# Performance work log

Hardware: AMD Instinct MI355X
Metric: run time of the kernel (lower is better)

Reference implementation:

```python
import jax, jax.numpy as jnp
import numpy as np
import math

B, SQ, SK, D = 16, 2048, 2048, 64


def setup_inputs() -> dict:
    key = jax.random.key(0)
    kq, kk, kv, kl = jax.random.split(key, 4)
    queries = jax.random.normal(kq, (B, SQ, D), dtype=jnp.float32)
    keys = jax.random.normal(kk, (B, SK, D), dtype=jnp.float32)
    values = jax.random.normal(kv, (B, SK, D), dtype=jnp.float32)
    # valid key lengths in [1, SK]
    valid_lens = jax.random.randint(kl, (B,), 1, SK + 1, dtype=jnp.int32)
    return {"queries": queries, "keys": keys, "values": values, "valid_lens": valid_lens}


def reference(queries, keys, values, valid_lens):
    d = queries.shape[-1]
    # [B, SQ, SK] raw scores
    scores = jnp.einsum("bqd,bkd->bqk", queries, keys) / math.sqrt(d)
    # masked_softmax: key positions >= valid_len are set to -1e6 (d2l semantics)
    kpos = jnp.arange(scores.shape[-1], dtype=jnp.int32)  # [SK]
    mask = kpos[None, None, :] < valid_lens[:, None, None]  # [B,1,SK] -> broadcast
    scores = jnp.where(mask, scores, jnp.float32(-1e6))
    attn = jax.nn.softmax(scores, axis=-1)
    # dropout rate is 0.0 -> identity
    return jnp.einsum("bqk,bkd->bqd", attn, values)
```

## Files before the change

kernel.cpp:

```cpp
#include <hip/hip_runtime.h>

#define NB 16
#define SQL 2048
#define SKL 2048
#define DH 64

typedef __attribute__((ext_vector_type(8))) short bf16x8;
typedef __attribute__((ext_vector_type(4))) unsigned short u16x4;
typedef __attribute__((ext_vector_type(8))) unsigned short u16x8;
typedef __attribute__((ext_vector_type(4))) float f32x4;

#define LOG2E 1.4426950408889634f
#define K1 (0.125f * LOG2E)

__device__ __forceinline__ unsigned short f2bf(float f) {
    unsigned int u = __builtin_bit_cast(unsigned int, f);
    u += 0x7fffu + ((u >> 16) & 1u);
    return (unsigned short)(u >> 16);
}

__global__ __launch_bounds__(256) void prep_kernel(
    const float* __restrict__ Q, const float* __restrict__ K,
    const float* __restrict__ V,
    unsigned short* __restrict__ Qb, unsigned short* __restrict__ Kb,
    unsigned short* __restrict__ Vt) {
    const int blk = blockIdx.x;
    if (blk < 2048) {
        const float* src = (blk < 1024) ? Q : K;
        unsigned short* dst = (blk < 1024) ? Qb : Kb;
        const size_t base = ((size_t)(blk & 1023) * 256 + threadIdx.x) * 8;
        float4 a = *(const float4*)(src + base);
        float4 b = *(const float4*)(src + base + 4);
        u16x8 o;
        o[0] = f2bf(a.x); o[1] = f2bf(a.y); o[2] = f2bf(a.z); o[3] = f2bf(a.w);
        o[4] = f2bf(b.x); o[5] = f2bf(b.y); o[6] = f2bf(b.z); o[7] = f2bf(b.w);
        *(u16x8*)(dst + base) = o;
    } else {
        const int t  = blk - 2048;
        const int b  = t >> 5;
        const int kb = (t & 31) << 6;
        __shared__ float tile[64][65];
        const int tid = threadIdx.x;
        {
            const int r  = tid >> 2;
            const int cg = (tid & 3) << 4;
            const float* vsrc = V + ((size_t)b * SKL + (kb + r)) * DH;
            #pragma unroll
            for (int i = 0; i < 4; ++i) {
                float4 x = *(const float4*)(vsrc + cg + i * 4);
                tile[r][cg + i*4 + 0] = x.x;
                tile[r][cg + i*4 + 1] = x.y;
                tile[r][cg + i*4 + 2] = x.z;
                tile[r][cg + i*4 + 3] = x.w;
            }
        }
        __syncthreads();
        {
            const int d  = tid >> 2;
            const int kg = (tid & 3) << 4;
            unsigned short* dst = Vt + ((size_t)b * DH + d) * SKL + kb + kg;
            u16x8 o0, o1;
            #pragma unroll
            for (int j = 0; j < 8; ++j) o0[j] = f2bf(tile[kg + j][d]);
            #pragma unroll
            for (int j = 0; j < 8; ++j) o1[j] = f2bf(tile[kg + 8 + j][d]);
            *(u16x8*)(dst)     = o0;
            *(u16x8*)(dst + 8) = o1;
        }
    }
}

__global__ __launch_bounds__(256, 2) void attn_kernel(
    const unsigned short* __restrict__ Qb,
    const unsigned short* __restrict__ Kb,
    const unsigned short* __restrict__ Vt,
    const int* __restrict__ valid_lens,
    float* __restrict__ out) {
    const int b    = blockIdx.y;
    const int qblk = blockIdx.x;
    const int tid  = threadIdx.x;
    const int wave = tid >> 6;
    const int lane = tid & 63;
    const int c16  = lane & 15;
    const int quad = lane >> 4;

    const int valid  = valid_lens[b];
    const int ntiles = (valid + 63) >> 6;

    __shared__ unsigned short Klds[64][72];
    __shared__ unsigned short Vlds[64][72];
    __shared__ unsigned short Plds[4][16][72];

    const int q0 = qblk * 64 + wave * 16;
    const unsigned short* qptr = Qb + ((size_t)b * SQL + q0 + c16) * DH;
    const bf16x8 qf0 = *(const bf16x8*)(qptr + quad * 8);
    const bf16x8 qf1 = *(const bf16x8*)(qptr + 32 + quad * 8);

    const unsigned short* kbase = Kb + (size_t)b * SKL * DH;
    const unsigned short* vbase = Vt + (size_t)b * DH * SKL;

    const f32x4 zero = {0.f, 0.f, 0.f, 0.f};
    f32x4 o[4];
    #pragma unroll
    for (int i = 0; i < 4; ++i) o[i] = zero;
    float mrow = -1e30f, lrow = 0.f;

    for (int kt = 0; kt < ntiles; ++kt) {
        const int kb = kt << 6;
        #pragma unroll
        for (int i = 0; i < 2; ++i) {
            const int c   = i * 256 + tid;
            const int r   = c >> 3;
            const int col = (c & 7) << 3;
            *(u16x8*)&Klds[r][col] = *(const u16x8*)(kbase + (size_t)(kb + r) * DH + col);
            *(u16x8*)&Vlds[r][col] = *(const u16x8*)(vbase + (size_t)r * SKL + kb + col);
        }
        __syncthreads();

        f32x4 s[4];
        #pragma unroll
        for (int t = 0; t < 4; ++t) {
            s[t] = zero;
            const bf16x8 kf0 = *(const bf16x8*)&Klds[t * 16 + c16][quad * 8];
            const bf16x8 kf1 = *(const bf16x8*)&Klds[t * 16 + c16][32 + quad * 8];
            s[t] = __builtin_amdgcn_mfma_f32_16x16x32_bf16(kf0, qf0, s[t], 0, 0, 0);
            s[t] = __builtin_amdgcn_mfma_f32_16x16x32_bf16(kf1, qf1, s[t], 0, 0, 0);
        }

        if (kb + 64 > valid) {
            #pragma unroll
            for (int t = 0; t < 4; ++t)
                #pragma unroll
                for (int r = 0; r < 4; ++r)
                    if (kb + t * 16 + quad * 4 + r >= valid) s[t][r] = -1e30f;
        }

        float tmax = -1e30f;
        #pragma unroll
        for (int t = 0; t < 4; ++t)
            #pragma unroll
            for (int r = 0; r < 4; ++r) tmax = fmaxf(tmax, s[t][r]);
        tmax = fmaxf(tmax, __shfl_xor(tmax, 16));
        tmax = fmaxf(tmax, __shfl_xor(tmax, 32));

        const float mnew  = fmaxf(mrow, 0.125f * tmax);
        const float alpha = exp2f((mrow - mnew) * LOG2E);
        const float mk    = mnew * LOG2E;
        float rs = 0.f;
        #pragma unroll
        for (int t = 0; t < 4; ++t)
            #pragma unroll
            for (int r = 0; r < 4; ++r) {
                const float p = exp2f(fmaf(s[t][r], K1, -mk));
                s[t][r] = p;
                rs += p;
            }
        rs += __shfl_xor(rs, 16);
        rs += __shfl_xor(rs, 32);
        lrow = lrow * alpha + rs;
        mrow = mnew;
        #pragma unroll
        for (int i = 0; i < 4; ++i) o[i] *= alpha;

        #pragma unroll
        for (int t = 0; t < 4; ++t) {
            u16x4 pw;
            pw[0] = f2bf(s[t][0]); pw[1] = f2bf(s[t][1]);
            pw[2] = f2bf(s[t][2]); pw[3] = f2bf(s[t][3]);
            *(u16x4*)&Plds[wave][c16][t * 16 + quad * 4] = pw;
        }
        const bf16x8 pf0 = *(const bf16x8*)&Plds[wave][c16][quad * 8];
        const bf16x8 pf1 = *(const bf16x8*)&Plds[wave][c16][32 + quad * 8];

        #pragma unroll
        for (int dt = 0; dt < 4; ++dt) {
            const bf16x8 vf0 = *(const bf16x8*)&Vlds[dt * 16 + c16][quad * 8];
            const bf16x8 vf1 = *(const bf16x8*)&Vlds[dt * 16 + c16][32 + quad * 8];
            o[dt] = __builtin_amdgcn_mfma_f32_16x16x32_bf16(vf0, pf0, o[dt], 0, 0, 0);
            o[dt] = __builtin_amdgcn_mfma_f32_16x16x32_bf16(vf1, pf1, o[dt], 0, 0, 0);
        }
        __syncthreads();
    }

    const float inv = 1.0f / lrow;
    float* op = out + ((size_t)b * SQL + q0 + c16) * DH + quad * 4;
    #pragma unroll
    for (int dt = 0; dt < 4; ++dt) {
        f32x4 ov = o[dt] * inv;
        *(f32x4*)(op + dt * 16) = ov;
    }
}

extern "C" void kernel_launch(void* const* d_in, const int* in_sizes, int n_in,
                              void* d_out, int out_size, void* d_ws, size_t ws_size,
                              hipStream_t stream) {
    const float* Q  = (const float*)d_in[0];
    const float* K  = (const float*)d_in[1];
    const float* V  = (const float*)d_in[2];
    const int*   vl = (const int*)d_in[3];
    float* out = (float*)d_out;

    unsigned short* Qb = (unsigned short*)d_ws;
    unsigned short* Kb = Qb + (size_t)NB * SQL * DH;
    unsigned short* Vt = Kb + (size_t)NB * SKL * DH;

    prep_kernel<<<dim3(2560), dim3(256), 0, stream>>>(Q, K, V, Qb, Kb, Vt);
    attn_kernel<<<dim3(SQL / 64, NB), dim3(256), 0, stream>>>(Qb, Kb, Vt, vl, out);
}
```

Baseline: 119.3 us.

## Split attention over key chunks with a separate reduce kernel, add prefetch and LDS swizzle

```diff
diff --git a/kernel.cpp b/kernel.cpp
--- a/kernel.cpp
+++ b/kernel.cpp
@@ -4,6 +4,8 @@
 #define SQL 2048
 #define SKL 2048
 #define DH 64
+#define NSPLIT 4
+#define CHUNK 512
 
 typedef __attribute__((ext_vector_type(8))) short bf16x8;
 typedef __attribute__((ext_vector_type(4))) unsigned short u16x4;
@@ -70,26 +72,33 @@
     }
 }
 
-__global__ __launch_bounds__(256, 2) void attn_kernel(
+__global__ __launch_bounds__(256, 4) void attn_kernel(
     const unsigned short* __restrict__ Qb,
     const unsigned short* __restrict__ Kb,
     const unsigned short* __restrict__ Vt,
     const int* __restrict__ valid_lens,
-    float* __restrict__ out) {
-    const int b    = blockIdx.y;
-    const int qblk = blockIdx.x;
+    float* __restrict__ Opart,
+    float2* __restrict__ MLpart) {
+    const int qblk  = blockIdx.x;
+    const int split = blockIdx.y;
+    const int b     = blockIdx.z;
+
+    const int valid  = valid_lens[b];
+    const int kstart = split * CHUNK;
+    if (kstart >= valid) return;
+    const int kend   = (valid < kstart + CHUNK) ? valid : (kstart + CHUNK);
+    const int ntiles = (kend - kstart + 63) >> 6;
+
     const int tid  = threadIdx.x;
     const int wave = tid >> 6;
     const int lane = tid & 63;
     const int c16  = lane & 15;
     const int quad = lane >> 4;
-
-    const int valid  = valid_lens[b];
-    const int ntiles = (valid + 63) >> 6;
-
-    __shared__ unsigned short Klds[64][72];
-    __shared__ unsigned short Vlds[64][72];
-    __shared__ unsigned short Plds[4][16][72];
+    const int h    = c16 & 7;
+
+    __shared__ unsigned short Klds[64][64];
+    __shared__ unsigned short Vlds[64][64];
+    __shared__ unsigned short Plds[4][16][64];
 
     const int q0 = qblk * 64 + wave * 16;
     const unsigned short* qptr = Qb + ((size_t)b * SQL + q0 + c16) * DH;
@@ -105,34 +114,53 @@
     for (int i = 0; i < 4; ++i) o[i] = zero;
     float mrow = -1e30f, lrow = 0.f;
 
+    u16x8 kreg[2], vreg[2];
+    {
+        #pragma unroll
+        for (int i = 0; i < 2; ++i) {
+            const int c = i * 256 + tid, r = c >> 3, col = (c & 7) << 3;
+            kreg[i] = *(const u16x8*)(kbase + (size_t)(kstart + r) * DH + col);
+            vreg[i] = *(const u16x8*)(vbase + (size_t)r * SKL + kstart + col);
+        }
+    }
+
     for (int kt = 0; kt < ntiles; ++kt) {
-        const int kb = kt << 6;
+        const int kb = kstart + (kt << 6);
+        __syncthreads();
         #pragma unroll
         for (int i = 0; i < 2; ++i) {
-            const int c   = i * 256 + tid;
-            const int r   = c >> 3;
-            const int col = (c & 7) << 3;
-            *(u16x8*)&Klds[r][col] = *(const u16x8*)(kbase + (size_t)(kb + r) * DH + col);
-            *(u16x8*)&Vlds[r][col] = *(const u16x8*)(vbase + (size_t)r * SKL + kb + col);
+            const int c = i * 256 + tid, r = c >> 3;
+            const int pc = ((c & 7) ^ (r & 7)) << 3;
+            *(u16x8*)&Klds[r][pc] = kreg[i];
+            *(u16x8*)&Vlds[r][pc] = vreg[i];
         }
         __syncthreads();
+        if (kt + 1 < ntiles) {
+            const int kn = kb + 64;
+            #pragma unroll
+            for (int i = 0; i < 2; ++i) {
+                const int c = i * 256 + tid, r = c >> 3, col = (c & 7) << 3;
+                kreg[i] = *(const u16x8*)(kbase + (size_t)(kn + r) * DH + col);
+                vreg[i] = *(const u16x8*)(vbase + (size_t)r * SKL + kn + col);
+            }
+        }
 
         f32x4 s[4];
         #pragma unroll
         for (int t = 0; t < 4; ++t) {
             s[t] = zero;
-            const bf16x8 kf0 = *(const bf16x8*)&Klds[t * 16 + c16][quad * 8];
-            const bf16x8 kf1 = *(const bf16x8*)&Klds[t * 16 + c16][32 + quad * 8];
+            const bf16x8 kf0 = *(const bf16x8*)&Klds[t*16 + c16][(quad       ^ h) << 3];
+            const bf16x8 kf1 = *(const bf16x8*)&Klds[t*16 + c16][((quad + 4) ^ h) << 3];
             s[t] = __builtin_amdgcn_mfma_f32_16x16x32_bf16(kf0, qf0, s[t], 0, 0, 0);
             s[t] = __builtin_amdgcn_mfma_f32_16x16x32_bf16(kf1, qf1, s[t], 0, 0, 0);
         }
 
-        if (kb + 64 > valid) {
+        if (kb + 64 > kend) {
             #pragma unroll
             for (int t = 0; t < 4; ++t)
                 #pragma unroll
                 for (int r = 0; r < 4; ++r)
-                    if (kb + t * 16 + quad * 4 + r >= valid) s[t][r] = -1e30f;
+                    if (kb + t * 16 + quad * 4 + r >= kend) s[t][r] = -1e30f;
         }
 
         float tmax = -1e30f;
@@ -167,28 +195,59 @@
             u16x4 pw;
             pw[0] = f2bf(s[t][0]); pw[1] = f2bf(s[t][1]);
             pw[2] = f2bf(s[t][2]); pw[3] = f2bf(s[t][3]);
-            *(u16x4*)&Plds[wave][c16][t * 16 + quad * 4] = pw;
-        }
-        const bf16x8 pf0 = *(const bf16x8*)&Plds[wave][c16][quad * 8];
-        const bf16x8 pf1 = *(const bf16x8*)&Plds[wave][c16][32 + quad * 8];
+            const int ch = 2 * t + (quad >> 1);
+            *(u16x4*)&Plds[wave][c16][((ch ^ h) << 3) + ((quad & 1) << 2)] = pw;
+        }
+        const bf16x8 pf0 = *(const bf16x8*)&Plds[wave][c16][(quad       ^ h) << 3];
+        const bf16x8 pf1 = *(const bf16x8*)&Plds[wave][c16][((quad + 4) ^ h) << 3];
 
         #pragma unroll
         for (int dt = 0; dt < 4; ++dt) {
-            const bf16x8 vf0 = *(const bf16x8*)&Vlds[dt * 16 + c16][quad * 8];
-            const bf16x8 vf1 = *(const bf16x8*)&Vlds[dt * 16 + c16][32 + quad * 8];
+            const bf16x8 vf0 = *(const bf16x8*)&Vlds[dt*16 + c16][(quad       ^ h) << 3];
+            const bf16x8 vf1 = *(const bf16x8*)&Vlds[dt*16 + c16][((quad + 4) ^ h) << 3];
             o[dt] = __builtin_amdgcn_mfma_f32_16x16x32_bf16(vf0, pf0, o[dt], 0, 0, 0);
             o[dt] = __builtin_amdgcn_mfma_f32_16x16x32_bf16(vf1, pf1, o[dt], 0, 0, 0);
         }
-        __syncthreads();
-    }
-
-    const float inv = 1.0f / lrow;
-    float* op = out + ((size_t)b * SQL + q0 + c16) * DH + quad * 4;
-    #pragma unroll
-    for (int dt = 0; dt < 4; ++dt) {
-        f32x4 ov = o[dt] * inv;
-        *(f32x4*)(op + dt * 16) = ov;
-    }
+    }
+
+    float* op = Opart + (((size_t)b * NSPLIT + split) * SQL + q0 + c16) * DH + quad * 4;
+    #pragma unroll
+    for (int dt = 0; dt < 4; ++dt) *(f32x4*)(op + dt * 16) = o[dt];
+    if (quad == 0)
+        MLpart[((size_t)b * NSPLIT + split) * SQL + q0 + c16] = make_float2(mrow, lrow);
+}
+
+__global__ __launch_bounds__(256) void reduce_kernel(
+    const float* __restrict__ Opart, const float2* __restrict__ MLpart,
+    const int* __restrict__ valid_lens, float* __restrict__ out) {
+    const int b   = blockIdx.y;
+    const int tid = threadIdx.x;
+    const int q   = blockIdx.x * 64 + (tid >> 2);
+    const int dg  = (tid & 3) << 4;
+    const int ns  = (valid_lens[b] + CHUNK - 1) / CHUNK;
+
+    float m[NSPLIT], l[NSPLIT];
+    float M = -1e30f;
+    for (int s = 0; s < ns; ++s) {
+        float2 ml = MLpart[((size_t)b * NSPLIT + s) * SQL + q];
+        m[s] = ml.x; l[s] = ml.y;
+        M = fmaxf(M, ml.x);
+    }
+    float L = 0.f;
+    f32x4 acc[4];
+    #pragma unroll
+    for (int i = 0; i < 4; ++i) acc[i] = (f32x4){0.f, 0.f, 0.f, 0.f};
+    for (int s = 0; s < ns; ++s) {
+        const float w = exp2f((m[s] - M) * LOG2E);
+        L += l[s] * w;
+        const float* p = Opart + (((size_t)b * NSPLIT + s) * SQL + q) * DH + dg;
+        #pragma unroll
+        for (int i = 0; i < 4; ++i) acc[i] += w * *(const f32x4*)(p + i * 4);
+    }
+    const float inv = 1.0f / L;
+    float* op = out + ((size_t)b * SQL + q) * DH + dg;
+    #pragma unroll
+    for (int i = 0; i < 4; ++i) *(f32x4*)(op + i * 4) = acc[i] * inv;
 }
 
 extern "C" void kernel_launch(void* const* d_in, const int* in_sizes, int n_in,
@@ -203,7 +262,12 @@
     unsigned short* Qb = (unsigned short*)d_ws;
     unsigned short* Kb = Qb + (size_t)NB * SQL * DH;
     unsigned short* Vt = Kb + (size_t)NB * SKL * DH;
+    float*  Opart  = (float*)(Vt + (size_t)NB * SKL * DH);
+    float2* MLpart = (float2*)(Opart + (size_t)NB * NSPLIT * SQL * DH);
 
     prep_kernel<<<dim3(2560), dim3(256), 0, stream>>>(Q, K, V, Qb, Kb, Vt);
-    attn_kernel<<<dim3(SQL / 64, NB), dim3(256), 0, stream>>>(Qb, Kb, Vt, vl, out);
-}
+    attn_kernel<<<dim3(SQL / 64, NSPLIT, NB), dim3(256), 0, stream>>>(
+        Qb, Kb, Vt, vl, Opart, MLpart);
+    reduce_kernel<<<dim3(SQL / 64, NB), dim3(256), 0, stream>>>(
+        Opart, MLpart, vl, out);
+}
```

Result: faster. 111.0 us (-7.0%).
